# Performance work log

Hardware: AMD Instinct MI355X
Metric: run time of the kernel (lower is better)

Reference implementation:

```python
import jax, jax.numpy as jnp
import numpy as np


def setup_inputs() -> dict:
    key = jax.random.key(0)
    k1, k2, k3, k4 = jax.random.split(key, 4)
    B, N, L, H, E = 2, 128, 128, 8, 64
    queries = jax.random.normal(k1, (B, N, L, H, E), dtype=jnp.float32)
    keys = jax.random.normal(k2, (B, N, L, H, E), dtype=jnp.float32)
    values = jax.random.normal(k3, (B, N, L, H, E), dtype=jnp.float32)
    # multiplicative spatial adjacency mask [B, N, M]
    attn_mask = jax.random.uniform(k4, (B, N, N), dtype=jnp.float32)
    return {"queries": queries, "keys": keys, "values": values, "attn_mask": attn_mask}


def reference(queries, keys, values, attn_mask):
    # queries/keys/values: [B, N, L, H, E]; attn_mask: [B, N, M]
    E = queries.shape[-1]
    scale = 1.0 / jnp.sqrt(jnp.asarray(E, queries.dtype))
    # --- temporal attention (per node, over time L) ---
    scores_t = jnp.einsum('bnlhe,bnshe->bnhls', queries, keys)  # [B,N,H,L,S]
    A_t = jax.nn.softmax(scale * scores_t, axis=-1)
    # dropout is identity at inference (Keras default training=False)
    V_t = jnp.einsum('bnhls,bnshd->bnlhd', A_t, values)  # [B,N,L,H,D]
    # --- spatial attention (per timestep, over nodes N) ---
    scores_s = jnp.einsum('bnlhe,bmlhe->blhnm', queries, keys)  # [B,L,H,N,M]
    scores_s = scores_s * attn_mask[:, None, None, :, :]        # multiplicative adjacency mask
    A_s = jax.nn.softmax(scale * scores_s, axis=-1)
    V = jnp.einsum('blhnm,bmlhd->bnlhd', A_s, V_t)  # [B,N,L,H,D]
    return V
```

## Files before the change

### kernel.cpp

```cpp
#include <hip/hip_runtime.h>

static constexpr int Bb = 2, Nn = 128, Ll = 128, Hh = 8, Ee = 64;
static constexpr float SCALE = 0.125f;

typedef short short8 __attribute__((ext_vector_type(8)));
typedef short short4v __attribute__((ext_vector_type(4)));
typedef float float4v __attribute__((ext_vector_type(4)));

#define MFMA16(a, b, c) __builtin_amdgcn_mfma_f32_16x16x32_bf16(a, b, c, 0, 0, 0)

__device__ inline float4 gload4(const float* p) {
  float4 r;
  asm volatile("global_load_dwordx4 %0, %1, off" : "=v"(r) : "v"(p) : "memory");
  return r;
}
__device__ inline float gload1(const float* p) {
  float r;
  asm volatile("global_load_dword %0, %1, off" : "=v"(r) : "v"(p) : "memory");
  return r;
}
#define WAIT_VM(N)                                        \
  do {                                                    \
    asm volatile("s_waitcnt vmcnt(" #N ")" ::: "memory"); \
    __builtin_amdgcn_sched_barrier(0);                    \
  } while (0)

__device__ inline unsigned short bf16_rne(float f) {
  unsigned u = __builtin_bit_cast(unsigned, f);
  u += 0x7FFFu + ((u >> 16) & 1u);
  return (unsigned short)(u >> 16);
}

__device__ inline void split4(float4 a, short4v& hi, short4v& lo) {
  float f[4] = {a.x, a.y, a.z, a.w};
#pragma unroll
  for (int j = 0; j < 4; ++j) {
    unsigned u = __builtin_bit_cast(unsigned, f[j]);
    unsigned short h = (unsigned short)(u >> 16);
    hi[j] = (short)h;
    float hf = __builtin_bit_cast(float, (unsigned)h << 16);
    lo[j] = (short)bf16_rne(f[j] - hf);
  }
}

__device__ inline void split8(float4 a, float4 b, short8& hi, short8& lo) {
  float f[8] = {a.x, a.y, a.z, a.w, b.x, b.y, b.z, b.w};
#pragma unroll
  for (int j = 0; j < 8; ++j) {
    unsigned u = __builtin_bit_cast(unsigned, f[j]);
    unsigned short h = (unsigned short)(u >> 16);
    hi[j] = (short)h;
    float hf = __builtin_bit_cast(float, (unsigned)h << 16);
    lo[j] = (short)bf16_rne(f[j] - hf);
  }
}

__device__ inline short8 pack4(const unsigned* p) {
  union { unsigned u[4]; short8 s; } t;
  t.u[0] = p[0]; t.u[1] = p[1]; t.u[2] = p[2]; t.u[3] = p[3];
  return t.s;
}

__device__ inline void lds_barrier() {
  __builtin_amdgcn_sched_barrier(0);
  asm volatile("s_waitcnt lgkmcnt(0)" ::: "memory");
  __builtin_amdgcn_s_barrier();
  __builtin_amdgcn_sched_barrier(0);
}

template <bool SPATIAL>
__global__ __launch_bounds__(512, 3) void st_attn(
    const float* __restrict__ Qp, const float* __restrict__ Kp,
    const void* __restrict__ Vp, const float* __restrict__ Mp,
    void* __restrict__ Op, int idx_stride, int row_stride) {
  __shared__ __align__(16) unsigned short Pb[128 * 130];
  __shared__ __align__(16) unsigned short Vb[64 * 130];

  const int g = blockIdx.x;
  const int b = g >> 10;
  const int idx = (g >> 3) & 127;
  const int h = g & 7;
  const int base = b * (Nn * Ll * Hh * Ee) + idx * idx_stride + h * Ee;

  const int tid = threadIdx.x;
  const int wave = tid >> 6;
  const int lane = tid & 63;
  const int tx = lane & 15;
  const int quad = lane >> 4;
  const int rowbase = wave * 16;
  const int rowb = rowbase + quad * 4;
  const int mb = b * (Nn * Nn);

  float4 kL[4], qL[4], vL[4];
  float mv[8][4];
#pragma unroll
  for (int it = 0; it < 4; ++it) {
    const int i4 = tid + it * 512;
    kL[it] = gload4(Kp + base + (i4 >> 4) * row_stride + ((i4 & 15) << 2));
  }
  {
    const float* qr = Qp + base + (rowbase + tx) * row_stride;
#pragma unroll
    for (int ks = 0; ks < 2; ++ks) {
      qL[ks * 2 + 0] = gload4(qr + ks * 32 + quad * 8);
      qL[ks * 2 + 1] = gload4(qr + ks * 32 + quad * 8 + 4);
    }
  }
  if constexpr (SPATIAL) {
    const unsigned short* Vt = (const unsigned short*)Vp;
    const unsigned short* vsl =
        Vt + ((b * Ll + idx) * Hh + h) * (Nn * Ee);
#pragma unroll
    for (int it = 0; it < 2; ++it) {
      const int i8 = tid + it * 512;
      vL[it] = gload4((const float*)(vsl + i8 * 8));
    }
#pragma unroll
    for (int ct = 0; ct < 8; ++ct)
#pragma unroll
      for (int e = 0; e < 4; ++e)
        mv[ct][e] = gload1(Mp + mb + (rowb + e) * 128 + ct * 16 + tx);
  } else {
    const float* Vf = (const float*)Vp;
#pragma unroll
    for (int it = 0; it < 4; ++it) {
      const int i4 = tid + it * 512;
      vL[it] = gload4(Vf + base + (i4 >> 4) * row_stride + ((i4 & 15) << 2));
    }
  }

  if constexpr (SPATIAL) WAIT_VM(34);
  else                   WAIT_VM(4);

#pragma unroll
  for (int it = 0; it < 4; ++it) {
    const int i4 = tid + it * 512;
    const int r = i4 >> 4;
    const int d0 = (i4 & 15) << 2;
    const int vs = d0 >> 3;
    const int idxk =
        ((((r >> 4) * 8 + vs) * 16 + (r & 15)) ^ vs) * 8 + (d0 & 7);
    short4v h4, l4;
    split4(kL[it], h4, l4);
    *(short4v*)(Pb + idxk) = h4;
    *(short4v*)(Pb + idxk + 8192) = l4;
  }

  short8 qhi[2], qlo[2];
#pragma unroll
  for (int ks = 0; ks < 2; ++ks)
    split8(qL[ks * 2 + 0], qL[ks * 2 + 1], qhi[ks], qlo[ks]);

  lds_barrier();

  float4v acc[8];
#pragma unroll
  for (int ct = 0; ct < 8; ++ct) acc[ct] = (float4v)(0.0f);

  const short8* KS8 = (const short8*)Pb;
#pragma unroll
  for (int ct = 0; ct < 8; ++ct) {
#pragma unroll
    for (int ks = 0; ks < 2; ++ks) {
      const int vs = ks * 4 + quad;
      const int fi = (((ct * 8 + vs) * 16 + tx) ^ vs);
      const short8 khi = KS8[fi];
      const short8 klo = KS8[fi + 1024];
      acc[ct] = MFMA16(qhi[ks], khi, acc[ct]);
      acc[ct] = MFMA16(qhi[ks], klo, acc[ct]);
      acc[ct] = MFMA16(qlo[ks], khi, acc[ct]);
    }
  }

  if constexpr (SPATIAL) WAIT_VM(0);

  float rowsum[4] = {0.f, 0.f, 0.f, 0.f};
#pragma unroll
  for (int ct = 0; ct < 8; ++ct) {
#pragma unroll
    for (int e = 0; e < 4; ++e) {
      float p = acc[ct][e] * SCALE;
      if (SPATIAL) p *= mv[ct][e];
      p = __expf(p);
      rowsum[e] += p;
      acc[ct][e] = p;
    }
  }

  float inv[4];
#pragma unroll
  for (int e = 0; e < 4; ++e) {
    float s = rowsum[e];
#pragma unroll
    for (int d = 1; d < 16; d <<= 1) s += __shfl_xor(s, d);
    inv[e] = 1.0f / s;
  }

  lds_barrier();

#pragma unroll
  for (int ct = 0; ct < 8; ++ct) {
    const int col = ct * 16 + tx;
#pragma unroll
    for (int e = 0; e < 4; ++e)
      Pb[(rowb + e) * 130 + col] = bf16_rne(acc[ct][e]);
  }

  if constexpr (SPATIAL) {
#pragma unroll
    for (int it = 0; it < 2; ++it) {
      const int i8 = tid + it * 512;
      const int m = i8 >> 3;
      const int e0 = (i8 & 7) * 8;
      union { float4 f; unsigned short u[8]; } t;
      t.f = vL[it];
#pragma unroll
      for (int j = 0; j < 8; ++j) Vb[(e0 + j) * 130 + m] = t.u[j];
    }
  } else {
    WAIT_VM(0);
#pragma unroll
    for (int it = 0; it < 4; ++it) {
      const int i4 = tid + it * 512;
      const int c = i4 >> 4;
      const int d0 = (i4 & 15) << 2;
      const float4 v = vL[it];
      Vb[(d0 + 0) * 130 + c] = bf16_rne(v.x);
      Vb[(d0 + 1) * 130 + c] = bf16_rne(v.y);
      Vb[(d0 + 2) * 130 + c] = bf16_rne(v.z);
      Vb[(d0 + 3) * 130 + c] = bf16_rne(v.w);
    }
  }

  __syncthreads();

  float4v accO[4];
#pragma unroll
  for (int dt = 0; dt < 4; ++dt) accO[dt] = (float4v)(0.0f);

#pragma unroll
  for (int ks = 0; ks < 4; ++ks) {
    const unsigned* pw =
        (const unsigned*)Pb + (rowbase + tx) * 65 + ks * 16 + quad * 4;
    const short8 pA = pack4(pw);
#pragma unroll
    for (int dt = 0; dt < 4; ++dt) {
      const unsigned* vw =
          (const unsigned*)Vb + (dt * 16 + tx) * 65 + ks * 16 + quad * 4;
      const short8 vB = pack4(vw);
      accO[dt] = MFMA16(pA, vB, accO[dt]);
    }
  }

  if constexpr (SPATIAL) {
    float* O = (float*)Op;
#pragma unroll
    for (int dt = 0; dt < 4; ++dt)
#pragma unroll
      for (int e = 0; e < 4; ++e)
        O[base + (rowb + e) * row_stride + dt * 16 + tx] =
            accO[dt][e] * inv[e];
  } else {
    unsigned short* O = (unsigned short*)Op;
#pragma unroll
    for (int dt = 0; dt < 4; ++dt)
#pragma unroll
      for (int e = 0; e < 4; ++e)
        O[((b * Ll + (rowb + e)) * Hh + h) * (Nn * Ee) + idx * Ee + dt * 16 +
          tx] = bf16_rne(accO[dt][e] * inv[e]);
  }
}

extern "C" void kernel_launch(void* const* d_in, const int* in_sizes, int n_in,
                              void* d_out, int out_size, void* d_ws,
                              size_t ws_size, hipStream_t stream) {
  const float* Q = (const float*)d_in[0];
  const float* K = (const float*)d_in[1];
  const float* V = (const float*)d_in[2];
  const float* M = (const float*)d_in[3];
  float* out = (float*)d_out;
  unsigned short* Vt = (unsigned short*)d_ws;

  dim3 grid(Bb * Nn * Hh), blk(512);
  st_attn<false><<<grid, blk, 0, stream>>>(Q, K, (const void*)V, nullptr,
                                           (void*)Vt, Ll * Hh * Ee ,
                                           Hh * Ee );
  st_attn<true><<<grid, blk, 0, stream>>>(Q, K, (const void*)Vt, M,
                                          (void*)out, Hh * Ee ,
                                          Ll * Hh * Ee );
}
```

Baseline: 264.7 us.

## Read K fragments directly from global and drop K staging in LDS

Each wave now loads its K fragments straight from global memory and splits them into hi/lo bf16 in registers, instead of staging split K in shared memory. The P buffer becomes per-wave, so the block-wide barriers before and after the score phase are replaced with a wave-local LDS fence. The inline-asm loads and hand-placed vmcnt waits are replaced with plain loads, and the occupancy hint goes from 3 to 4 blocks. In exchange, every wave re-reads all 128 K rows from global/L2 (eight times the K traffic per block), and the V staging and its barrier now sit before the Q/K math, so that latency is no longer overlapped with compute.

```diff
diff --git a/kernel.cpp b/kernel.cpp
--- a/kernel.cpp
+++ b/kernel.cpp
@@ -4,43 +4,14 @@
 static constexpr float SCALE = 0.125f;
 
 typedef short short8 __attribute__((ext_vector_type(8)));
-typedef short short4v __attribute__((ext_vector_type(4)));
 typedef float float4v __attribute__((ext_vector_type(4)));
 
 #define MFMA16(a, b, c) __builtin_amdgcn_mfma_f32_16x16x32_bf16(a, b, c, 0, 0, 0)
-
-__device__ inline float4 gload4(const float* p) {
-  float4 r;
-  asm volatile("global_load_dwordx4 %0, %1, off" : "=v"(r) : "v"(p) : "memory");
-  return r;
-}
-__device__ inline float gload1(const float* p) {
-  float r;
-  asm volatile("global_load_dword %0, %1, off" : "=v"(r) : "v"(p) : "memory");
-  return r;
-}
-#define WAIT_VM(N)                                        \
-  do {                                                    \
-    asm volatile("s_waitcnt vmcnt(" #N ")" ::: "memory"); \
-    __builtin_amdgcn_sched_barrier(0);                    \
-  } while (0)
 
 __device__ inline unsigned short bf16_rne(float f) {
   unsigned u = __builtin_bit_cast(unsigned, f);
   u += 0x7FFFu + ((u >> 16) & 1u);
   return (unsigned short)(u >> 16);
-}
-
-__device__ inline void split4(float4 a, short4v& hi, short4v& lo) {
-  float f[4] = {a.x, a.y, a.z, a.w};
-#pragma unroll
-  for (int j = 0; j < 4; ++j) {
-    unsigned u = __builtin_bit_cast(unsigned, f[j]);
-    unsigned short h = (unsigned short)(u >> 16);
-    hi[j] = (short)h;
-    float hf = __builtin_bit_cast(float, (unsigned)h << 16);
-    lo[j] = (short)bf16_rne(f[j] - hf);
-  }
 }
 
 __device__ inline void split8(float4 a, float4 b, short8& hi, short8& lo) {
@@ -61,19 +32,18 @@
   return t.s;
 }
 
-__device__ inline void lds_barrier() {
+__device__ inline void wave_lds_fence() {
   __builtin_amdgcn_sched_barrier(0);
   asm volatile("s_waitcnt lgkmcnt(0)" ::: "memory");
-  __builtin_amdgcn_s_barrier();
   __builtin_amdgcn_sched_barrier(0);
 }
 
 template <bool SPATIAL>
-__global__ __launch_bounds__(512, 3) void st_attn(
+__global__ __launch_bounds__(512, 4) void st_attn(
     const float* __restrict__ Qp, const float* __restrict__ Kp,
     const void* __restrict__ Vp, const float* __restrict__ Mp,
     void* __restrict__ Op, int idx_stride, int row_stride) {
-  __shared__ __align__(16) unsigned short Pb[128 * 130];
+  __shared__ __align__(16) unsigned short Pb[8 * 16 * 130];
   __shared__ __align__(16) unsigned short Vb[64 * 130];
 
   const int g = blockIdx.x;
@@ -91,140 +61,27 @@
   const int rowb = rowbase + quad * 4;
   const int mb = b * (Nn * Nn);
 
-  float4 kL[4], qL[4], vL[4];
-  float mv[8][4];
-#pragma unroll
-  for (int it = 0; it < 4; ++it) {
-    const int i4 = tid + it * 512;
-    kL[it] = gload4(Kp + base + (i4 >> 4) * row_stride + ((i4 & 15) << 2));
-  }
-  {
-    const float* qr = Qp + base + (rowbase + tx) * row_stride;
-#pragma unroll
-    for (int ks = 0; ks < 2; ++ks) {
-      qL[ks * 2 + 0] = gload4(qr + ks * 32 + quad * 8);
-      qL[ks * 2 + 1] = gload4(qr + ks * 32 + quad * 8 + 4);
-    }
-  }
   if constexpr (SPATIAL) {
-    const unsigned short* Vt = (const unsigned short*)Vp;
     const unsigned short* vsl =
-        Vt + ((b * Ll + idx) * Hh + h) * (Nn * Ee);
+        (const unsigned short*)Vp + ((b * Ll + idx) * Hh + h) * (Nn * Ee);
 #pragma unroll
     for (int it = 0; it < 2; ++it) {
       const int i8 = tid + it * 512;
-      vL[it] = gload4((const float*)(vsl + i8 * 8));
-    }
-#pragma unroll
-    for (int ct = 0; ct < 8; ++ct)
-#pragma unroll
-      for (int e = 0; e < 4; ++e)
-        mv[ct][e] = gload1(Mp + mb + (rowb + e) * 128 + ct * 16 + tx);
+      union { float4 f; unsigned short u[8]; } t;
+      t.f = *(const float4*)(vsl + i8 * 8);
+      const int m = i8 >> 3;
+      const int e0 = (i8 & 7) * 8;
+#pragma unroll
+      for (int j = 0; j < 8; ++j) Vb[(e0 + j) * 130 + m] = t.u[j];
+    }
   } else {
     const float* Vf = (const float*)Vp;
-#pragma unroll
-    for (int it = 0; it < 4; ++it) {
-      const int i4 = tid + it * 512;
-      vL[it] = gload4(Vf + base + (i4 >> 4) * row_stride + ((i4 & 15) << 2));
-    }
-  }
-
-  if constexpr (SPATIAL) WAIT_VM(34);
-  else                   WAIT_VM(4);
-
-#pragma unroll
-  for (int it = 0; it < 4; ++it) {
-    const int i4 = tid + it * 512;
-    const int r = i4 >> 4;
-    const int d0 = (i4 & 15) << 2;
-    const int vs = d0 >> 3;
-    const int idxk =
-        ((((r >> 4) * 8 + vs) * 16 + (r & 15)) ^ vs) * 8 + (d0 & 7);
-    short4v h4, l4;
-    split4(kL[it], h4, l4);
-    *(short4v*)(Pb + idxk) = h4;
-    *(short4v*)(Pb + idxk + 8192) = l4;
-  }
-
-  short8 qhi[2], qlo[2];
-#pragma unroll
-  for (int ks = 0; ks < 2; ++ks)
-    split8(qL[ks * 2 + 0], qL[ks * 2 + 1], qhi[ks], qlo[ks]);
-
-  lds_barrier();
-
-  float4v acc[8];
-#pragma unroll
-  for (int ct = 0; ct < 8; ++ct) acc[ct] = (float4v)(0.0f);
-
-  const short8* KS8 = (const short8*)Pb;
-#pragma unroll
-  for (int ct = 0; ct < 8; ++ct) {
-#pragma unroll
-    for (int ks = 0; ks < 2; ++ks) {
-      const int vs = ks * 4 + quad;
-      const int fi = (((ct * 8 + vs) * 16 + tx) ^ vs);
-      const short8 khi = KS8[fi];
-      const short8 klo = KS8[fi + 1024];
-      acc[ct] = MFMA16(qhi[ks], khi, acc[ct]);
-      acc[ct] = MFMA16(qhi[ks], klo, acc[ct]);
-      acc[ct] = MFMA16(qlo[ks], khi, acc[ct]);
-    }
-  }
-
-  if constexpr (SPATIAL) WAIT_VM(0);
-
-  float rowsum[4] = {0.f, 0.f, 0.f, 0.f};
-#pragma unroll
-  for (int ct = 0; ct < 8; ++ct) {
-#pragma unroll
-    for (int e = 0; e < 4; ++e) {
-      float p = acc[ct][e] * SCALE;
-      if (SPATIAL) p *= mv[ct][e];
-      p = __expf(p);
-      rowsum[e] += p;
-      acc[ct][e] = p;
-    }
-  }
-
-  float inv[4];
-#pragma unroll
-  for (int e = 0; e < 4; ++e) {
-    float s = rowsum[e];
-#pragma unroll
-    for (int d = 1; d < 16; d <<= 1) s += __shfl_xor(s, d);
-    inv[e] = 1.0f / s;
-  }
-
-  lds_barrier();
-
-#pragma unroll
-  for (int ct = 0; ct < 8; ++ct) {
-    const int col = ct * 16 + tx;
-#pragma unroll
-    for (int e = 0; e < 4; ++e)
-      Pb[(rowb + e) * 130 + col] = bf16_rne(acc[ct][e]);
-  }
-
-  if constexpr (SPATIAL) {
-#pragma unroll
-    for (int it = 0; it < 2; ++it) {
-      const int i8 = tid + it * 512;
-      const int m = i8 >> 3;
-      const int e0 = (i8 & 7) * 8;
-      union { float4 f; unsigned short u[8]; } t;
-      t.f = vL[it];
-#pragma unroll
-      for (int j = 0; j < 8; ++j) Vb[(e0 + j) * 130 + m] = t.u[j];
-    }
-  } else {
-    WAIT_VM(0);
 #pragma unroll
     for (int it = 0; it < 4; ++it) {
       const int i4 = tid + it * 512;
       const int c = i4 >> 4;
       const int d0 = (i4 & 15) << 2;
-      const float4 v = vL[it];
+      const float4 v = *(const float4*)(Vf + base + c * row_stride + d0);
       Vb[(d0 + 0) * 130 + c] = bf16_rne(v.x);
       Vb[(d0 + 1) * 130 + c] = bf16_rne(v.y);
       Vb[(d0 + 2) * 130 + c] = bf16_rne(v.z);
@@ -234,20 +91,87 @@
 
   __syncthreads();
 
+  short8 qhi[2], qlo[2];
+  {
+    const float* qr = Qp + base + (rowbase + tx) * row_stride;
+#pragma unroll
+    for (int ks = 0; ks < 2; ++ks) {
+      const float4 a = *(const float4*)(qr + ks * 32 + quad * 8);
+      const float4 c = *(const float4*)(qr + ks * 32 + quad * 8 + 4);
+      split8(a, c, qhi[ks], qlo[ks]);
+    }
+  }
+
+  float4v acc[8];
+#pragma unroll
+  for (int ct = 0; ct < 8; ++ct) acc[ct] = (float4v)(0.0f);
+
+#pragma unroll
+  for (int ct = 0; ct < 8; ++ct) {
+    const float* kr = Kp + base + (ct * 16 + tx) * row_stride;
+#pragma unroll
+    for (int ks = 0; ks < 2; ++ks) {
+      const float4 a = *(const float4*)(kr + ks * 32 + quad * 8);
+      const float4 c = *(const float4*)(kr + ks * 32 + quad * 8 + 4);
+      short8 khi, klo;
+      split8(a, c, khi, klo);
+      acc[ct] = MFMA16(qhi[ks], khi, acc[ct]);
+      acc[ct] = MFMA16(qhi[ks], klo, acc[ct]);
+      acc[ct] = MFMA16(qlo[ks], khi, acc[ct]);
+    }
+  }
+
+  float rowsum[4] = {0.f, 0.f, 0.f, 0.f};
+#pragma unroll
+  for (int ct = 0; ct < 8; ++ct) {
+    float mv[4];
+    if constexpr (SPATIAL) {
+#pragma unroll
+      for (int e = 0; e < 4; ++e)
+        mv[e] = Mp[mb + (rowb + e) * 128 + ct * 16 + tx];
+    }
+#pragma unroll
+    for (int e = 0; e < 4; ++e) {
+      float p = acc[ct][e] * SCALE;
+      if (SPATIAL) p *= mv[e];
+      p = __expf(p);
+      rowsum[e] += p;
+      acc[ct][e] = p;
+    }
+  }
+
+  float inv[4];
+#pragma unroll
+  for (int e = 0; e < 4; ++e) {
+    float s = rowsum[e];
+#pragma unroll
+    for (int d = 1; d < 16; d <<= 1) s += __shfl_xor(s, d);
+    inv[e] = 1.0f / s;
+  }
+
+  unsigned short* myP = Pb + wave * (16 * 130);
+#pragma unroll
+  for (int ct = 0; ct < 8; ++ct) {
+    const int col = ct * 16 + tx;
+#pragma unroll
+    for (int e = 0; e < 4; ++e)
+      myP[(quad * 4 + e) * 130 + col] = bf16_rne(acc[ct][e]);
+  }
+
+  wave_lds_fence();
+
   float4v accO[4];
 #pragma unroll
   for (int dt = 0; dt < 4; ++dt) accO[dt] = (float4v)(0.0f);
 
 #pragma unroll
   for (int ks = 0; ks < 4; ++ks) {
-    const unsigned* pw =
-        (const unsigned*)Pb + (rowbase + tx) * 65 + ks * 16 + quad * 4;
-    const short8 pA = pack4(pw);
+    const short8 pA =
+        pack4((const unsigned*)myP + tx * 65 + ks * 16 + quad * 4);
 #pragma unroll
     for (int dt = 0; dt < 4; ++dt) {
-      const unsigned* vw =
-          (const unsigned*)Vb + (dt * 16 + tx) * 65 + ks * 16 + quad * 4;
-      const short8 vB = pack4(vw);
+      const short8 vB =
+          pack4((const unsigned*)Vb + (dt * 16 + tx) * 65 + ks * 16 + quad * 4);
       accO[dt] = MFMA16(pA, vB, accO[dt]);
     }
   }
```

After: 338.6 us. +27.9%, slower.
